# Kernel optimization log

Hardware: AMD Instinct MI355X
Metric: run time of the kernel (lower is better)

## Reference

```python
import jax, jax.numpy as jnp
import numpy as np

# hyperparameters from init_kwargs
TEMP = 0.05
MOMENTUM = 0.2
ALPHA = 0.9
TEMP_DIST = 0.6
LAMBDA1 = 1.0
LAMBDA2 = 1.0
EPS_CONS = 2.0
NUM_SAMPLES = 8192
NUM_FEATURES = 2048
B = 256
K = 20
EPS = 1e-12


def setup_inputs() -> dict:
    key = jax.random.key(0)
    ks = jax.random.split(key, 8)
    inputs0 = jax.random.normal(ks[0], (B, NUM_FEATURES), dtype=jnp.float32)
    logits0 = jax.random.normal(ks[1], (B, NUM_SAMPLES), dtype=jnp.float32)
    logits1 = jax.random.normal(ks[2], (B, NUM_SAMPLES), dtype=jnp.float32)
    targets = jax.random.randint(ks[3], (B,), 0, NUM_SAMPLES, dtype=jnp.int32)
    indexes = jnp.arange(B, dtype=jnp.int32)  # global idx == batch idx (identity idx2bidx)
    neighbors = jax.random.randint(ks[4], (B, K), 0, B, dtype=jnp.int32)
    neighbor_dists = jax.random.uniform(ks[5], (B, K), dtype=jnp.float32)
    rampup = jnp.ones((), dtype=jnp.float32)
    features = jax.random.normal(ks[6], (NUM_SAMPLES, NUM_FEATURES), dtype=jnp.float32)
    features = features / jnp.linalg.norm(features, axis=1, keepdims=True)
    return {
        'inputs0': inputs0, 'logits0': logits0, 'logits1': logits1,
        'targets': targets, 'indexes': indexes, 'neighbors': neighbors,
        'neighbor_dists': neighbor_dists, 'rampup': rampup, 'features': features,
    }


def reference(inputs0, logits0, logits1, targets, indexes, neighbors,
              neighbor_dists, rampup, features):
    # F.normalize(inputs[0], dim=1)
    x = inputs0 / jnp.maximum(jnp.linalg.norm(inputs0, axis=1, keepdims=True), EPS)

    # CM forward: scores against memory bank, scaled by temperature
    outputs = (x @ features.T) / TEMP                      # [B, S]
    logp = jax.nn.log_softmax(outputs, axis=-1)
    loss_nce = -jnp.mean(jnp.take_along_axis(logp, targets[:, None], axis=1))

    targets_onehot = jax.nn.one_hot(targets, NUM_SAMPLES, dtype=logits0.dtype)

    # neighbor gathering: indexes = arange(B) so idx2bidx is identity; every
    # neighbor in [0,B) passes the `nb in indexes` filter.
    p0 = jax.nn.softmax(logits0, axis=-1)[neighbors]       # [B, K, S]
    p1 = jax.nn.softmax(logits1, axis=-1)[neighbors]       # [B, K, S]
    # loop appends logits0-row then logits1-row per neighbor -> interleave
    p = jnp.stack([p0, p1], axis=2).reshape(B, 2 * K, NUM_SAMPLES)
    d2 = jnp.repeat(neighbor_dists, 2, axis=1)             # [B, 2K] (d,d pairs)
    w = jax.nn.softmax(d2 / TEMP_DIST, axis=1)             # [B, 2K]
    logits_neighbors1 = jnp.einsum('bk,bks->bs', w, p)     # [B, S]

    # KL branch: neighbors with dist <= eps_consistency (all, since eps=2.0)
    mask = (neighbor_dists <= EPS_CONS).astype(p0.dtype)   # [B, K]
    cnt = jnp.maximum(mask.sum(axis=1, keepdims=True), 1.0)
    logits_neighbors1_KL = jnp.einsum('bk,bks->bs', mask, p0) / cnt  # [B, S]

    refined = ALPHA * targets_onehot + (1.0 - ALPHA) * jax.lax.stop_gradient(logits_neighbors1)
    loss_ce = jnp.mean(jnp.sum(-refined * jax.nn.log_softmax(logits0, axis=-1), axis=1))

    # KLDivLoss(logsoftmax(logits1).detach(), target) with batchmean reduction
    lp1 = jax.lax.stop_gradient(jax.nn.log_softmax(logits1, axis=-1))
    t = logits_neighbors1_KL
    kl = jnp.sum(jnp.where(t > 0, t * (jnp.log(jnp.maximum(t, EPS)) - lp1), 0.0)) / B

    # CM momentum memory-bank scatter update (backward side-effect in torch);
    # equivalent to the sequential loop when targets are unique in the batch.
    upd = MOMENTUM * features[targets] + (1.0 - MOMENTUM) * x
    upd = upd / jnp.maximum(jnp.linalg.norm(upd, axis=1, keepdims=True), EPS)
    new_features = features.at[targets].set(upd)

    return (loss_nce, LAMBDA1 * loss_ce, LAMBDA2 * rampup * kl, new_features)
```

## Files before the change

kernel.cpp:

```cpp
#include <hip/hip_runtime.h>
#include <cmath>

#define NB 256
#define NS 8192
#define NF 2048
#define NK 20

typedef _Float16 half8 __attribute__((ext_vector_type(8)));
typedef _Float16 half4 __attribute__((ext_vector_type(4)));
typedef float f32x4 __attribute__((ext_vector_type(4)));

__device__ __forceinline__ void async16(const void* g, void* l) {
  __builtin_amdgcn_global_load_lds(
      (const __attribute__((address_space(1))) unsigned int*)g,
      (__attribute__((address_space(3))) unsigned int*)l, 16, 0, 0);
}

__device__ __forceinline__ float waveSum(float v) {
#pragma unroll
  for (int off = 32; off > 0; off >>= 1) v += __shfl_xor(v, off, 64);
  return v;
}
__device__ __forceinline__ float waveMax(float v) {
#pragma unroll
  for (int off = 32; off > 0; off >>= 1) v = fmaxf(v, __shfl_xor(v, off, 64));
  return v;
}

__global__ __launch_bounds__(256, 1) void prep(
    const float4* __restrict__ f4, const float* __restrict__ in0,
    const float* __restrict__ logits0, const float* __restrict__ logits1,
    const int* __restrict__ targets, const int* __restrict__ neighbors,
    const float* __restrict__ ndist,
    float* __restrict__ outF, _Float16* __restrict__ fh,
    _Float16* __restrict__ Pt, _Float16* __restrict__ xh,
    _Float16* __restrict__ alpha_h, float* __restrict__ mll,
    _Float16* __restrict__ Wp) {
  __shared__ alignas(16) union {
    struct {
      float redA[4];
      float redB[4];
      unsigned long long wmask[4];
    } s;
    _Float16 Lt[32 * 520];
  } sm;
  int tid = threadIdx.x, blk = blockIdx.x;
  int wave = tid >> 6, lane = tid & 63;

  if (blk < NS) {
    int row = blk;
    const float4* fr = f4 + (size_t)row * (NF / 4);
    float4 v0 = fr[tid], v1 = fr[tid + 256];
    half4 h0, h1;
    h0[0] = (_Float16)v0.x; h0[1] = (_Float16)v0.y; h0[2] = (_Float16)v0.z; h0[3] = (_Float16)v0.w;
    h1[0] = (_Float16)v1.x; h1[1] = (_Float16)v1.y; h1[2] = (_Float16)v1.z; h1[3] = (_Float16)v1.w;
    ((half4*)(fh + (size_t)row * NF))[tid] = h0;
    ((half4*)(fh + (size_t)row * NF))[tid + 256] = h1;
    unsigned long long mk = __ballot(targets[tid] == row);
    if (lane == 0) sm.s.wmask[wave] = mk;
    __syncthreads();
    int u = -1;
#pragma unroll
    for (int w = 3; w >= 0; --w)
      if (u < 0 && sm.s.wmask[w])
        u = w * 64 + 63 - (int)__clzll(sm.s.wmask[w]);
    if (u >= 0) {
      const float4* xr = (const float4*)(in0 + (size_t)u * NF);
      float4 a0 = xr[tid], a1 = xr[tid + 256];
      float ssx = a0.x * a0.x + a0.y * a0.y + a0.z * a0.z + a0.w * a0.w +
                  a1.x * a1.x + a1.y * a1.y + a1.z * a1.z + a1.w * a1.w;
      float w1 = waveSum(ssx);
      if (lane == 0) sm.s.redA[wave] = w1;
      __syncthreads();
      float totx = (sm.s.redA[0] + sm.s.redA[1]) + (sm.s.redA[2] + sm.s.redA[3]);
      float ix = 0.8f / fmaxf(sqrtf(totx), 1e-12f);
      v0 = make_float4(0.2f * v0.x + ix * a0.x, 0.2f * v0.y + ix * a0.y,
                       0.2f * v0.z + ix * a0.z, 0.2f * v0.w + ix * a0.w);
      v1 = make_float4(0.2f * v1.x + ix * a1.x, 0.2f * v1.y + ix * a1.y,
                       0.2f * v1.z + ix * a1.z, 0.2f * v1.w + ix * a1.w);
      float ss = v0.x * v0.x + v0.y * v0.y + v0.z * v0.z + v0.w * v0.w +
                 v1.x * v1.x + v1.y * v1.y + v1.z * v1.z + v1.w * v1.w;
      float w2 = waveSum(ss);
      if (lane == 0) sm.s.redB[wave] = w2;
      __syncthreads();
      float tot = (sm.s.redB[0] + sm.s.redB[1]) + (sm.s.redB[2] + sm.s.redB[3]);
      float inv = 1.0f / fmaxf(sqrtf(tot), 1e-12f);
      v0.x *= inv; v0.y *= inv; v0.z *= inv; v0.w *= inv;
      v1.x *= inv; v1.y *= inv; v1.z *= inv; v1.w *= inv;
    }
    float* o = outF + (size_t)row * NF;
    int e0 = tid * 4, e1 = 1024 + tid * 4;
    o[e0 + 0] = v0.x; o[e0 + 1] = v0.y; o[e0 + 2] = v0.z; o[e0 + 3] = v0.w;
    o[e1 + 0] = v1.x; o[e1 + 1] = v1.y; o[e1 + 2] = v1.z; o[e1 + 3] = v1.w;
  } else if (blk < NS + 512) {
    int r = blk - NS;
    const float* src = (r < NB) ? logits0 : logits1;
    const float4* row = (const float4*)(src + (size_t)(r & (NB - 1)) * NS);
    float4 v[8];
    float mx = -1e30f;
#pragma unroll
    for (int i = 0; i < 8; ++i) {
      v[i] = row[tid + i * 256];
      mx = fmaxf(mx, fmaxf(fmaxf(v[i].x, v[i].y), fmaxf(v[i].z, v[i].w)));
    }
    float wv = waveMax(mx);
    if (lane == 0) sm.s.redA[wave] = wv;
    __syncthreads();
    float m = fmaxf(fmaxf(sm.s.redA[0], sm.s.redA[1]), fmaxf(sm.s.redA[2], sm.s.redA[3]));
    float se = 0.0f;
#pragma unroll
    for (int i = 0; i < 8; ++i)
      se += expf(v[i].x - m) + expf(v[i].y - m) + expf(v[i].z - m) + expf(v[i].w - m);
    float sw = waveSum(se);
    if (lane == 0) sm.s.redB[wave] = sw;
    __syncthreads();
    float l = (sm.s.redB[0] + sm.s.redB[1]) + (sm.s.redB[2] + sm.s.redB[3]);
    if (tid == 0) {
      mll[r] = m + logf(l);
      alpha_h[r] = (_Float16)(256.0f * expf(-m) / l);
    }
  } else if (blk < NS + 768) {
    int s0 = (blk - (NS + 512)) * 32;
#pragma unroll
    for (int g = 0; g < 16; ++g) {
      int pos = g * 256 + tid;
      int row = pos >> 3, c4 = pos & 7;
      const float* src = ((row < NB) ? logits0 + (size_t)row * NS
                                     : logits1 + (size_t)(row - NB) * NS) + s0 + c4 * 4;
      float4 v = *(const float4*)src;
      sm.Lt[(c4 * 4 + 0) * 520 + row] = (_Float16)expf(v.x);
      sm.Lt[(c4 * 4 + 1) * 520 + row] = (_Float16)expf(v.y);
      sm.Lt[(c4 * 4 + 2) * 520 + row] = (_Float16)expf(v.z);
      sm.Lt[(c4 * 4 + 3) * 520 + row] = (_Float16)expf(v.w);
    }
    __syncthreads();
    int srow = tid >> 3, seg = tid & 7;
    _Float16* dst = Pt + (size_t)(s0 + srow) * 512 + seg * 64;
    const _Float16* lsrc = &sm.Lt[srow * 520 + seg * 64];
#pragma unroll
    for (int q = 0; q < 8; ++q)
      *(half8*)(dst + q * 8) = *(const half8*)(lsrc + q * 8);
  } else if (blk < NS + 1024) {
    int b = blk - (NS + 768);
    const float4* row = (const float4*)(in0 + (size_t)b * NF);
    float4 v0 = row[tid], v1 = row[tid + 256];
    float ss = v0.x * v0.x + v0.y * v0.y + v0.z * v0.z + v0.w * v0.w +
               v1.x * v1.x + v1.y * v1.y + v1.z * v1.z + v1.w * v1.w;
    float w = waveSum(ss);
    if (lane == 0) sm.s.redA[wave] = w;
    __syncthreads();
    float tot = (sm.s.redA[0] + sm.s.redA[1]) + (sm.s.redA[2] + sm.s.redA[3]);
    float inv = 1.0f / fmaxf(sqrtf(tot), 1e-12f);
    half4 h0, h1;
    h0[0] = (_Float16)(v0.x * inv); h0[1] = (_Float16)(v0.y * inv);
    h0[2] = (_Float16)(v0.z * inv); h0[3] = (_Float16)(v0.w * inv);
    h1[0] = (_Float16)(v1.x * inv); h1[1] = (_Float16)(v1.y * inv);
    h1[2] = (_Float16)(v1.z * inv); h1[3] = (_Float16)(v1.w * inv);
    ((half4*)(xh + (size_t)b * NF))[tid] = h0;
    ((half4*)(xh + (size_t)b * NF))[tid + 256] = h1;
  } else {
    float4* W4 = (float4*)Wp;
    for (int i = tid; i < 512 * 512 * 2 / 16; i += 256) W4[i] = make_float4(0, 0, 0, 0);
    __syncthreads();
    int b = tid;
    float d[NK], e[NK];
    int n[NK];
    float s = 0.0f;
    int cnt = 0;
#pragma unroll
    for (int k = 0; k < NK; ++k) {
      d[k] = ndist[b * NK + k];
      n[k] = neighbors[b * NK + k];
      e[k] = expf(d[k] * (1.0f / 0.6f));
      s += e[k];
      cnt += (d[k] <= 2.0f) ? 1 : 0;
    }
    float invs = 1.0f / (2.0f * s);
    float invc = 1.0f / fmaxf((float)cnt, 1.0f);
    _Float16* rkl = Wp + (size_t)b * 512;
    _Float16* rce = Wp + (size_t)(256 + b) * 512;
#pragma unroll
    for (int k = 0; k < NK; ++k) {
      bool first = true;
#pragma unroll
      for (int k2 = 0; k2 < NK; ++k2)
        if (k2 < k && n[k2] == n[k]) first = false;
      if (first) {
        float wsum = 0.0f, ksum = 0.0f;
#pragma unroll
        for (int k2 = 0; k2 < NK; ++k2)
          if (k2 >= k && n[k2] == n[k]) {
            wsum += e[k2] * invs;
            ksum += (d[k2] <= 2.0f) ? invc : 0.0f;
          }
        rkl[n[k]] = (_Float16)ksum;
        rce[n[k]] = (_Float16)wsum;
        rce[256 + n[k]] = (_Float16)wsum;
      }
    }
  }
}

__global__ __launch_bounds__(256) void gemms(
    const _Float16* __restrict__ xh, const _Float16* __restrict__ fh,
    const _Float16* __restrict__ Wp, const _Float16* __restrict__ Pt,
    const _Float16* __restrict__ alpha_h,
    const float* __restrict__ logits0, const float* __restrict__ logits1,
    const float* __restrict__ mll, const int* __restrict__ targets,
    float* __restrict__ pm, float* __restrict__ pl, float* __restrict__ tgt,
    float* __restrict__ part) {
  __shared__ alignas(16) _Float16 As[128 * 64];
  __shared__ alignas(16) _Float16 Bs[128 * 64];
  __shared__ alignas(16) _Float16 Al[512];
  __shared__ float red[4];
  int tid = threadIdx.x, wave = tid >> 6, lane = tid & 63;
  int quad = lane >> 4, r16 = lane & 15, lrow = lane >> 3, lch = lane & 7;
  int blk = blockIdx.x;
  if (blk < 256) {
    int bx = blk & 127, by = blk >> 7;
    int n0 = bx * 64, m0 = by * 128;
    f32x4 acc[2][4] = {};
    for (int k0 = 0; k0 < NF; k0 += 64) {
      __syncthreads();
#pragma unroll
      for (int ss = 0; ss < 4; ++ss) {
        int rl = ss * 32 + wave * 8 + lrow;
        int sc = lch ^ (rl & 7);
        async16(xh + (size_t)(m0 + rl) * NF + k0 + sc * 8, &As[rl * 64 + lch * 8]);
      }
#pragma unroll
      for (int ss = 0; ss < 2; ++ss) {
        int rl = ss * 32 + wave * 8 + lrow;
        int sc = lch ^ (rl & 7);
        async16(fh + (size_t)(n0 + rl) * NF + k0 + sc * 8, &Bs[rl * 64 + lch * 8]);
      }
      __syncthreads();
#pragma unroll
      for (int sub = 0; sub < 2; ++sub) {
        int slot = ((sub * 4 + quad) ^ (r16 & 7)) * 8;
        half8 af[2], bf[4];
#pragma unroll
        for (int i = 0; i < 2; ++i)
          af[i] = *(const half8*)&As[(wave * 32 + i * 16 + r16) * 64 + slot];
#pragma unroll
        for (int j = 0; j < 4; ++j)
          bf[j] = *(const half8*)&Bs[(j * 16 + r16) * 64 + slot];
#pragma unroll
        for (int i = 0; i < 2; ++i)
#pragma unroll
          for (int j = 0; j < 4; ++j)
            acc[i][j] = __builtin_amdgcn_mfma_f32_16x16x32_f16(af[i], bf[j], acc[i][j], 0, 0, 0);
      }
    }
#pragma unroll
    for (int i = 0; i < 2; ++i)
#pragma unroll
      for (int r = 0; r < 4; ++r) {
        int R = m0 + wave * 32 + i * 16 + quad * 4 + r;
        float sv[4];
#pragma unroll
        for (int j = 0; j < 4; ++j) sv[j] = acc[i][j][r] * 20.0f;
        float mx = fmaxf(fmaxf(sv[0], sv[1]), fmaxf(sv[2], sv[3]));
#pragma unroll
        for (int m2 = 1; m2 < 16; m2 <<= 1) mx = fmaxf(mx, __shfl_xor(mx, m2, 64));
        float e = expf(sv[0] - mx) + expf(sv[1] - mx) + expf(sv[2] - mx) + expf(sv[3] - mx);
#pragma unroll
        for (int m2 = 1; m2 < 16; m2 <<= 1) e += __shfl_xor(e, m2, 64);
        int tg = targets[R];
#pragma unroll
        for (int j = 0; j < 4; ++j)
          if (n0 + j * 16 + r16 == tg) tgt[R] = sv[j];
        if (r16 == 0) { pm[R * 128 + bx] = mx; pl[R * 128 + bx] = e; }
      }
  } else {
    int nb = blk - 256;
    int bx = nb & 63, by = nb >> 6;
    int n0 = bx * 128, m0 = by * 128;
    int wm = (wave >> 1) * 64, wn = (wave & 1) * 64;
    if (tid < 64) ((half8*)Al)[tid] = ((const half8*)alpha_h)[tid];
    f32x4 acc[4][4] = {};
    for (int k0 = 0; k0 < 512; k0 += 64) {
      __syncthreads();
#pragma unroll
      for (int ss = 0; ss < 4; ++ss) {
        int rl = ss * 32 + wave * 8 + lrow;
        int sc = lch ^ (rl & 7);
        async16(Wp + (size_t)(m0 + rl) * 512 + k0 + sc * 8, &As[rl * 64 + lch * 8]);
        async16(Pt + (size_t)(n0 + rl) * 512 + k0 + sc * 8, &Bs[rl * 64 + lch * 8]);
      }
      __syncthreads();
#pragma unroll
      for (int sub = 0; sub < 2; ++sub) {
        int slot = ((sub * 4 + quad) ^ (r16 & 7)) * 8;
        half8 alv = *(const half8*)&Al[k0 + slot];
        half8 af[4], bf[4];
#pragma unroll
        for (int i = 0; i < 4; ++i)
          af[i] = *(const half8*)&As[(wm + i * 16 + r16) * 64 + slot];
#pragma unroll
        for (int j = 0; j < 4; ++j)
          bf[j] = *(const half8*)&Bs[(wn + j * 16 + r16) * 64 + slot] * alv;
#pragma unroll
        for (int i = 0; i < 4; ++i)
#pragma unroll
          for (int j = 0; j < 4; ++j)
            acc[i][j] = __builtin_amdgcn_mfma_f32_16x16x32_f16(af[i], bf[j], acc[i][j], 0, 0, 0);
      }
    }
    bool iskl = (by < 2);
    const float* lgbase = iskl ? logits1 : logits0;
    float local = 0.0f;
#pragma unroll
    for (int i = 0; i < 4; ++i)
#pragma unroll
      for (int r = 0; r < 4; ++r) {
        int Mg = m0 + wm + i * 16 + quad * 4 + r;
        int b = iskl ? Mg : (Mg - 256);
        float mv = mll[iskl ? 256 + b : b];
        const float* lgrow = lgbase + (size_t)b * NS + n0 + wn;
#pragma unroll
        for (int j = 0; j < 4; ++j) {
          float lg = lgrow[j * 16 + r16];
          float t = acc[i][j][r] * (1.0f / 256.0f);
          if (iskl)
            local += (t > 0.0f) ? t * (logf(fmaxf(t, 1e-12f)) - (lg - mv)) : 0.0f;
          else
            local += -0.1f * t * (lg - mv);
        }
      }
    float wsv = waveSum(local);
    if (lane == 0) red[wave] = wsv;
    __syncthreads();
    if (tid == 0) part[nb] = (red[0] + red[1]) + (red[2] + red[3]);
  }
}

__global__ __launch_bounds__(256) void final_reduce(
    const float* __restrict__ pm, const float* __restrict__ pl,
    const float* __restrict__ tgt, const float* __restrict__ part,
    const float* __restrict__ logits0, const float* __restrict__ mll,
    const int* __restrict__ targets, const float* __restrict__ rampup,
    float* __restrict__ out) {
  __shared__ float rA[4], rB[4], rC[4], rD[4];
  int tid = threadIdx.x, wave = tid >> 6, lane = tid & 63;
  int b = tid;
  const float* pmb = pm + b * 128;
  const float* plb = pl + b * 128;
  float mx = -1e30f;
  for (int s = 0; s < 128; ++s) mx = fmaxf(mx, pmb[s]);
  float S = 0.0f;
  for (int s = 0; s < 128; ++s) S += plb[s] * expf(pmb[s] - mx);
  float nce = -(tgt[b] - mx - logf(S));
  int tg = targets[b];
  float oh = -0.9f * (logits0[(size_t)b * NS + tg] - mll[b]);
  float c = part[tid];
  float klc = (tid < 128) ? c : 0.0f;
  float cec = (tid < 128) ? 0.0f : c;
  float wn_ = waveSum(nce), wo = waveSum(oh), wk = waveSum(klc), wc = waveSum(cec);
  if (lane == 0) { rA[wave] = wn_; rB[wave] = wo; rC[wave] = wk; rD[wave] = wc; }
  __syncthreads();
  if (tid == 0) {
    float sn = rA[0] + rA[1] + rA[2] + rA[3];
    float so = rB[0] + rB[1] + rB[2] + rB[3];
    float sk = rC[0] + rC[1] + rC[2] + rC[3];
    float sc2 = rD[0] + rD[1] + rD[2] + rD[3];
    out[0] = sn * (1.0f / 256.0f);
    out[1] = (so + sc2) * (1.0f / 256.0f);
    out[2] = rampup[0] * sk * (1.0f / 256.0f);
  }
}

extern "C" void kernel_launch(void* const* d_in, const int* in_sizes, int n_in,
                              void* d_out, int out_size, void* d_ws, size_t ws_size,
                              hipStream_t stream) {
  const float* inputs0 = (const float*)d_in[0];
  const float* logits0 = (const float*)d_in[1];
  const float* logits1 = (const float*)d_in[2];
  const int* targets = (const int*)d_in[3];
  const int* neighbors = (const int*)d_in[5];
  const float* ndist = (const float*)d_in[6];
  const float* rampup = (const float*)d_in[7];
  const float* features = (const float*)d_in[8];
  float* out = (float*)d_out;

  char* ws = (char*)d_ws;
  float* mll = (float*)(ws + 4096);
  _Float16* alpha_h = (_Float16*)(ws + 8192);
  float* part = (float*)(ws + 12288);
  float* tgt = (float*)(ws + 16384);
  float* pm = (float*)(ws + 65536);
  float* pl = (float*)(ws + 196608);
  _Float16* Wp = (_Float16*)(ws + 524288);
  _Float16* xh = (_Float16*)(ws + (3 << 20));
  _Float16* Pt = (_Float16*)(ws + (4 << 20));
  _Float16* fh = (_Float16*)(ws + (12 << 20));

  prep<<<NS + 1025, 256, 0, stream>>>((const float4*)features, inputs0, logits0,
                                      logits1, targets, neighbors, ndist,
                                      out + 3, fh, Pt, xh, alpha_h, mll, Wp);
  gemms<<<512, 256, 0, stream>>>(xh, fh, Wp, Pt, alpha_h, logits0, logits1, mll,
                                 targets, pm, pl, tgt, part);
  final_reduce<<<1, 256, 0, stream>>>(pm, pl, tgt, part, logits0, mll, targets,
                                      rampup, out);
}
```

Measured before the change: 223.0 us.

## Fuse final reduction into GEMM kernel via last-block counter; vectorize misaligned stores

The separate single-block final_reduce launch is removed. The last-finishing GEMM block, found through an agent-scope atomic counter that prep resets, now does the final reduction. This saves one kernel launch and its gap. The memory-bank output is at out+3, so it is misaligned by one float. Its stores are rewritten as float4 writes shifted by one element, using a lane shuffle, instead of scalar stores. The transposed softmax-exp staging now uses 16 columns per block instead of 32, doubling the block count and halving LDS per block.

```diff
diff --git a/kernel.cpp b/kernel.cpp
--- a/kernel.cpp
+++ b/kernel.cpp
@@ -35,14 +35,14 @@
     float* __restrict__ outF, _Float16* __restrict__ fh,
     _Float16* __restrict__ Pt, _Float16* __restrict__ xh,
     _Float16* __restrict__ alpha_h, float* __restrict__ mll,
-    _Float16* __restrict__ Wp) {
+    _Float16* __restrict__ Wp, int* __restrict__ cnt) {
   __shared__ alignas(16) union {
     struct {
       float redA[4];
       float redB[4];
       unsigned long long wmask[4];
     } s;
-    _Float16 Lt[32 * 520];
+    _Float16 Lt[16 * 520];
   } sm;
   int tid = threadIdx.x, blk = blockIdx.x;
   int wave = tid >> 6, lane = tid & 63;
@@ -89,9 +89,16 @@
       v1.x *= inv; v1.y *= inv; v1.z *= inv; v1.w *= inv;
     }
     float* o = outF + (size_t)row * NF;
-    int e0 = tid * 4, e1 = 1024 + tid * 4;
-    o[e0 + 0] = v0.x; o[e0 + 1] = v0.y; o[e0 + 2] = v0.z; o[e0 + 3] = v0.w;
-    o[e1 + 0] = v1.x; o[e1 + 1] = v1.y; o[e1 + 2] = v1.z; o[e1 + 3] = v1.w;
+    float n0x = __shfl_down(v0.x, 1, 64);
+    float n1x = __shfl_down(v1.x, 1, 64);
+    if (lane != 63) {
+      *(float4*)(o + 4 * tid + 1) = make_float4(v0.y, v0.z, v0.w, n0x);
+      *(float4*)(o + 1024 + 4 * tid + 1) = make_float4(v1.y, v1.z, v1.w, n1x);
+    } else {
+      o[4 * tid + 1] = v0.y; o[4 * tid + 2] = v0.z; o[4 * tid + 3] = v0.w;
+      o[1024 + 4 * tid + 1] = v1.y; o[1024 + 4 * tid + 2] = v1.z; o[1024 + 4 * tid + 3] = v1.w;
+    }
+    if (lane == 0) { o[4 * tid] = v0.x; o[1024 + 4 * tid] = v1.x; }
   } else if (blk < NS + 512) {
     int r = blk - NS;
     const float* src = (r < NB) ? logits0 : logits1;
@@ -119,12 +126,12 @@
       mll[r] = m + logf(l);
       alpha_h[r] = (_Float16)(256.0f * expf(-m) / l);
     }
-  } else if (blk < NS + 768) {
-    int s0 = (blk - (NS + 512)) * 32;
-#pragma unroll
-    for (int g = 0; g < 16; ++g) {
+  } else if (blk < NS + 1024) {
+    int s0 = (blk - (NS + 512)) * 16;
+#pragma unroll
+    for (int g = 0; g < 8; ++g) {
       int pos = g * 256 + tid;
-      int row = pos >> 3, c4 = pos & 7;
+      int row = pos >> 2, c4 = pos & 3;
       const float* src = ((row < NB) ? logits0 + (size_t)row * NS
                                      : logits1 + (size_t)(row - NB) * NS) + s0 + c4 * 4;
       float4 v = *(const float4*)src;
@@ -134,14 +141,14 @@
       sm.Lt[(c4 * 4 + 3) * 520 + row] = (_Float16)expf(v.w);
     }
     __syncthreads();
-    int srow = tid >> 3, seg = tid & 7;
-    _Float16* dst = Pt + (size_t)(s0 + srow) * 512 + seg * 64;
-    const _Float16* lsrc = &sm.Lt[srow * 520 + seg * 64];
-#pragma unroll
-    for (int q = 0; q < 8; ++q)
+    int srow = tid >> 4, seg = tid & 15;
+    _Float16* dst = Pt + (size_t)(s0 + srow) * 512 + seg * 32;
+    const _Float16* lsrc = &sm.Lt[srow * 520 + seg * 32];
+#pragma unroll
+    for (int q = 0; q < 4; ++q)
       *(half8*)(dst + q * 8) = *(const half8*)(lsrc + q * 8);
-  } else if (blk < NS + 1024) {
-    int b = blk - (NS + 768);
+  } else if (blk < NS + 1280) {
+    int b = blk - (NS + 1024);
     const float4* row = (const float4*)(in0 + (size_t)b * NF);
     float4 v0 = row[tid], v1 = row[tid + 256];
     float ss = v0.x * v0.x + v0.y * v0.y + v0.z * v0.z + v0.w * v0.w +
@@ -161,22 +168,23 @@
   } else {
     float4* W4 = (float4*)Wp;
     for (int i = tid; i < 512 * 512 * 2 / 16; i += 256) W4[i] = make_float4(0, 0, 0, 0);
+    if (tid == 0) *cnt = 0;
     __syncthreads();
     int b = tid;
     float d[NK], e[NK];
     int n[NK];
     float s = 0.0f;
-    int cnt = 0;
+    int c2 = 0;
 #pragma unroll
     for (int k = 0; k < NK; ++k) {
       d[k] = ndist[b * NK + k];
       n[k] = neighbors[b * NK + k];
       e[k] = expf(d[k] * (1.0f / 0.6f));
       s += e[k];
-      cnt += (d[k] <= 2.0f) ? 1 : 0;
+      c2 += (d[k] <= 2.0f) ? 1 : 0;
     }
     float invs = 1.0f / (2.0f * s);
-    float invc = 1.0f / fmaxf((float)cnt, 1.0f);
+    float invc = 1.0f / fmaxf((float)c2, 1.0f);
     _Float16* rkl = Wp + (size_t)b * 512;
     _Float16* rce = Wp + (size_t)(256 + b) * 512;
 #pragma unroll
@@ -207,12 +215,14 @@
     const _Float16* __restrict__ alpha_h,
     const float* __restrict__ logits0, const float* __restrict__ logits1,
     const float* __restrict__ mll, const int* __restrict__ targets,
+    const float* __restrict__ rampup,
     float* __restrict__ pm, float* __restrict__ pl, float* __restrict__ tgt,
-    float* __restrict__ part) {
+    float* __restrict__ part, int* cnt, float* __restrict__ out) {
   __shared__ alignas(16) _Float16 As[128 * 64];
   __shared__ alignas(16) _Float16 Bs[128 * 64];
   __shared__ alignas(16) _Float16 Al[512];
   __shared__ float red[4];
+  __shared__ int lastFlag;
   int tid = threadIdx.x, wave = tid >> 6, lane = tid & 63;
   int quad = lane >> 4, r16 = lane & 15, lrow = lane >> 3, lch = lane & 7;
   int blk = blockIdx.x;
@@ -333,22 +343,25 @@
     __syncthreads();
     if (tid == 0) part[nb] = (red[0] + red[1]) + (red[2] + red[3]);
   }
-}
-
-__global__ __launch_bounds__(256) void final_reduce(
-    const float* __restrict__ pm, const float* __restrict__ pl,
-    const float* __restrict__ tgt, const float* __restrict__ part,
-    const float* __restrict__ logits0, const float* __restrict__ mll,
-    const int* __restrict__ targets, const float* __restrict__ rampup,
-    float* __restrict__ out) {
+
+  __syncthreads();
+  if (tid == 0) {
+    int prev = __hip_atomic_fetch_add(cnt, 1, __ATOMIC_ACQ_REL, __HIP_MEMORY_SCOPE_AGENT);
+    lastFlag = (prev == 511);
+  }
+  __syncthreads();
+  if (!lastFlag) return;
+  __threadfence();
+
   __shared__ float rA[4], rB[4], rC[4], rD[4];
-  int tid = threadIdx.x, wave = tid >> 6, lane = tid & 63;
   int b = tid;
   const float* pmb = pm + b * 128;
   const float* plb = pl + b * 128;
   float mx = -1e30f;
+#pragma unroll 8
   for (int s = 0; s < 128; ++s) mx = fmaxf(mx, pmb[s]);
   float S = 0.0f;
+#pragma unroll 8
   for (int s = 0; s < 128; ++s) S += plb[s] * expf(pmb[s] - mx);
   float nce = -(tgt[b] - mx - logf(S));
   int tg = targets[b];
@@ -388,6 +401,7 @@
   _Float16* alpha_h = (_Float16*)(ws + 8192);
   float* part = (float*)(ws + 12288);
   float* tgt = (float*)(ws + 16384);
+  int* cnt = (int*)(ws + 20480);
   float* pm = (float*)(ws + 65536);
   float* pl = (float*)(ws + 196608);
   _Float16* Wp = (_Float16*)(ws + 524288);
@@ -395,11 +409,9 @@
   _Float16* Pt = (_Float16*)(ws + (4 << 20));
   _Float16* fh = (_Float16*)(ws + (12 << 20));
 
-  prep<<<NS + 1025, 256, 0, stream>>>((const float4*)features, inputs0, logits0,
+  prep<<<NS + 1281, 256, 0, stream>>>((const float4*)features, inputs0, logits0,
                                       logits1, targets, neighbors, ndist,
-                                      out + 3, fh, Pt, xh, alpha_h, mll, Wp);
+                                      out + 3, fh, Pt, xh, alpha_h, mll, Wp, cnt);
   gemms<<<512, 256, 0, stream>>>(xh, fh, Wp, Pt, alpha_h, logits0, logits1, mll,
-                                 targets, pm, pl, tgt, part);
-  final_reduce<<<1, 256, 0, stream>>>(pm, pl, tgt, part, logits0, mll, targets,
-                                      rampup, out);
-}
+                                 targets, rampup, pm, pl, tgt, part, cnt, out);
+}
```

After: 233.0 us. 1.04x slower.
